# Performance work log

Hardware: AMD Instinct MI355X
Metric: run time of the kernel (lower is better)

## Reference

```python
import jax, jax.numpy as jnp
import numpy as np

B, C, H, W = 4, 256, 48, 48
NUM_HEADS = 8
HEAD_DIM = C // NUM_HEADS
LN_EPS = 1e-5


def setup_inputs() -> dict:
    key = jax.random.key(0)
    ks = jax.random.split(key, 12)
    s = 1.0 / np.sqrt(C)
    return {
        "x": jax.random.normal(ks[0], (B, C, H, W), dtype=jnp.float32),
        "context": jax.random.normal(ks[1], (B, C, H, W), dtype=jnp.float32),
        "Wq": jax.random.uniform(ks[2], (C, C), jnp.float32, -s, s),
        "bq": jax.random.uniform(ks[3], (C,), jnp.float32, -s, s),
        "Wk": jax.random.uniform(ks[4], (C, C), jnp.float32, -s, s),
        "bk": jax.random.uniform(ks[5], (C,), jnp.float32, -s, s),
        "Wv": jax.random.uniform(ks[6], (C, C), jnp.float32, -s, s),
        "bv": jax.random.uniform(ks[7], (C,), jnp.float32, -s, s),
        "Wo": jax.random.uniform(ks[8], (C, C), jnp.float32, -s, s),
        "bo": jax.random.uniform(ks[9], (C,), jnp.float32, -s, s),
        "ln_w": jnp.ones((C,), jnp.float32),
        "ln_b": jnp.zeros((C,), jnp.float32),
    }


def reference(x, context, Wq, bq, Wk, bk, Wv, bv, Wo, bo, ln_w, ln_b):
    b, c, h, w = x.shape
    S = h * w
    # [B, S, C] token layout (x.view(B,C,-1).permute(0,2,1))
    x_flat = x.reshape(b, c, S).transpose(0, 2, 1)
    ctx_flat = context.reshape(b, c, S).transpose(0, 2, 1)
    # QKV projections (torch Linear: y = x @ W.T + b)
    q = (x_flat @ Wq.T + bq).reshape(b, S, NUM_HEADS, HEAD_DIM).transpose(0, 2, 1, 3)
    k = (ctx_flat @ Wk.T + bk).reshape(b, S, NUM_HEADS, HEAD_DIM).transpose(0, 2, 1, 3)
    v = (ctx_flat @ Wv.T + bv).reshape(b, S, NUM_HEADS, HEAD_DIM).transpose(0, 2, 1, 3)
    # attention: [B, heads, S, S]
    scores = jnp.einsum("bhqd,bhkd->bhqk", q, k) / np.sqrt(HEAD_DIM)
    attn = jax.nn.softmax(scores, axis=-1)  # dropout is identity in eval mode
    attended = jnp.einsum("bhqk,bhkd->bhqd", attn, v)
    attended = attended.transpose(0, 2, 1, 3).reshape(b, S, c)
    out = attended @ Wo.T + bo
    # residual + layernorm over channel dim
    y = out + x_flat
    mu = jnp.mean(y, axis=-1, keepdims=True)
    var = jnp.var(y, axis=-1, keepdims=True)
    y = (y - mu) * jax.lax.rsqrt(var + LN_EPS) * ln_w + ln_b
    return y.transpose(0, 2, 1).reshape(b, c, h, w)
```

## Files before the change

kernel.cpp:

```cpp
#include <hip/hip_runtime.h>

#define B_ 4
#define C_ 256
#define S_ 2304
#define NH_ 8
#define HD_ 32
#define QS_L2E (0.17677669529663687f * 1.4426950408889634f)

typedef __attribute__((ext_vector_type(8))) __bf16 b16x8;
typedef __attribute__((ext_vector_type(4))) __bf16 b16x4;
typedef __attribute__((ext_vector_type(4))) float f32x4;

static __device__ __forceinline__ f32x4 mfma_bf16(b16x8 a, b16x8 b, f32x4 c) {
  return __builtin_amdgcn_mfma_f32_16x16x32_bf16(a, b, c, 0, 0, 0);
}

__global__ __launch_bounds__(256) void k_cvt(
    const float* __restrict__ x, const float* __restrict__ ctx,
    const float* __restrict__ Wq, const float* __restrict__ Wk,
    const float* __restrict__ Wv, const float* __restrict__ Wo,
    __bf16* __restrict__ xT, __bf16* __restrict__ cT,
    __bf16* __restrict__ Wb, __bf16* __restrict__ Wob) {
  const int bid = blockIdx.x, t = threadIdx.x;
  if (bid < 1152) {
    __shared__ float tile[32][33];
    const int tr = t >> 3, tc = (t & 7) * 4;
#pragma unroll
    for (int i = 0; i < 4; ++i) {
      const int tid4 = bid * 4 + i;
      const int s = tid4 / 2304;
      int r = tid4 % 2304;
      const int b = r / 576; r %= 576;
      const int ct = r / 72, st = r % 72;
      const float* src = (s == 0 ? x : ctx) + ((size_t)b * C_ + ct * 32) * S_ + st * 32;
      if (i) __syncthreads();
      f32x4 v = *(const f32x4*)(src + (size_t)tr * S_ + tc);
      tile[tr][tc] = v[0]; tile[tr][tc + 1] = v[1];
      tile[tr][tc + 2] = v[2]; tile[tr][tc + 3] = v[3];
      __syncthreads();
      __bf16* dst = (s == 0 ? xT : cT) + ((size_t)b * S_ + st * 32 + tr) * C_ + ct * 32 + tc;
      b16x4 o;
#pragma unroll
      for (int j = 0; j < 4; ++j) o[j] = (__bf16)tile[tc + j][tr];
      *(b16x4*)dst = o;
    }
  } else {
    const int bid2 = bid - 1152;
#pragma unroll
    for (int i = 0; i < 4; ++i) {
      const int wi = bid2 * 4 + i;
      const int m = wi >> 6, chunk = wi & 63;
      const float* Wsrc = m == 0 ? Wq : (m == 1 ? Wk : (m == 2 ? Wv : Wo));
      __bf16* Wdst = (m < 3) ? (Wb + m * 65536) : Wob;
      const int e0 = chunk * 1024 + t * 4;
      f32x4 v = *(const f32x4*)(Wsrc + e0);
      b16x4 o;
#pragma unroll
      for (int j = 0; j < 4; ++j) o[j] = (__bf16)v[j];
      *(b16x4*)(Wdst + e0) = o;
    }
  }
}

__global__ __launch_bounds__(256) void k_qkv(
    const __bf16* __restrict__ xT, const __bf16* __restrict__ cT,
    const __bf16* __restrict__ Wb,
    const float* __restrict__ bq, const float* __restrict__ bk, const float* __restrict__ bv,
    __bf16* __restrict__ Q, __bf16* __restrict__ Kd, __bf16* __restrict__ Vt) {
  const int iblk = threadIdx.x >> 6;
  const int lane = threadIdx.x & 63;
  const int col = lane & 15, g = lane >> 4;
  int r = blockIdx.x;
  const int p = r / 288; r %= 288;
  const int b = r / 72;
  const int s0 = (r % 72) * 32;
  const __bf16* src = (p == 0 ? xT : cT) + (size_t)b * S_ * C_;
  const __bf16* W = Wb + p * 65536;
  const float* bias = p == 0 ? bq : (p == 1 ? bk : bv);
  const int i0 = iblk * 64;

  f32x4 acc[2][4] = {};
  const __bf16* brow0 = src + (size_t)(s0 + col) * C_ + g * 8;
  const __bf16* brow1 = brow0 + 16 * C_;
  const __bf16* arow = W + (size_t)(i0 + col) * C_ + g * 8;

  b16x8 bf0 = *(const b16x8*)(brow0);
  b16x8 bf1 = *(const b16x8*)(brow1);
  b16x8 af0 = *(const b16x8*)(arow);
  b16x8 af1 = *(const b16x8*)(arow + (size_t)16 * C_);
  b16x8 af2 = *(const b16x8*)(arow + (size_t)32 * C_);
  b16x8 af3 = *(const b16x8*)(arow + (size_t)48 * C_);

  for (int kk = 0; kk < 8; ++kk) {
    const int nk = (kk + 1) * 32;
    b16x8 nbf0 = *(const b16x8*)(brow0 + nk);
    b16x8 nbf1 = *(const b16x8*)(brow1 + nk);
    b16x8 naf0 = *(const b16x8*)(arow + nk);
    b16x8 naf1 = *(const b16x8*)(arow + (size_t)16 * C_ + nk);
    b16x8 naf2 = *(const b16x8*)(arow + (size_t)32 * C_ + nk);
    b16x8 naf3 = *(const b16x8*)(arow + (size_t)48 * C_ + nk);
    __builtin_amdgcn_sched_barrier(0);
    acc[0][0] = mfma_bf16(af0, bf0, acc[0][0]);
    acc[0][1] = mfma_bf16(af1, bf0, acc[0][1]);
    acc[0][2] = mfma_bf16(af2, bf0, acc[0][2]);
    acc[0][3] = mfma_bf16(af3, bf0, acc[0][3]);
    acc[1][0] = mfma_bf16(af0, bf1, acc[1][0]);
    acc[1][1] = mfma_bf16(af1, bf1, acc[1][1]);
    acc[1][2] = mfma_bf16(af2, bf1, acc[1][2]);
    acc[1][3] = mfma_bf16(af3, bf1, acc[1][3]);
    bf0 = nbf0; bf1 = nbf1; af0 = naf0; af1 = naf1; af2 = naf2; af3 = naf3;
  }
#pragma unroll
  for (int tf = 0; tf < 2; ++tf) {
#pragma unroll
    for (int j = 0; j < 4; ++j) {
#pragma unroll
      for (int rr = 0; rr < 4; ++rr) {
        const int i = i0 + j * 16 + g * 4 + rr;
        float val = acc[tf][j][rr] + bias[i];
        const int h = i >> 5, d = i & 31;
        const size_t bh = (size_t)b * NH_ + h;
        const int tok = s0 + tf * 16 + col;
        if (p == 0)      Q[(bh * S_ + tok) * HD_ + d] = (__bf16)(val * QS_L2E);
        else if (p == 1) Kd[(bh * S_ + tok) * HD_ + d] = (__bf16)val;
        else             Vt[(bh * HD_ + d) * S_ + tok] = (__bf16)val;
      }
    }
  }
}

__global__ __launch_bounds__(192) void k_attn(
    const __bf16* __restrict__ Q, const __bf16* __restrict__ Kd,
    const __bf16* __restrict__ Vt, __bf16* __restrict__ att) {
  __shared__ float mrg[2][4][528];
  int bid = blockIdx.x;
  bid = (bid & 7) * 144 + (bid >> 3);
  const int wid = threadIdx.x >> 6;
  const int lane = threadIdx.x & 63;
  const int col = lane & 15, g = lane >> 4;
  const int bh = bid / 36;
  const int s0 = (bid % 36) * 64;
  const int b = bh >> 3, h = bh & 7;
  const __bf16* Qb = Q + (size_t)bh * S_ * HD_;
  const __bf16* Kb = Kd + (size_t)bh * S_ * HD_;
  const __bf16* Vb = Vt + (size_t)bh * HD_ * S_;

  b16x8 qfr[4];
#pragma unroll
  for (int q = 0; q < 4; ++q)
    qfr[q] = *(const b16x8*)(Qb + (size_t)(s0 + q * 16 + col) * HD_ + g * 8);
  const int kA = ((col >> 2) * 8) + (col & 3);
  const int kbeg = wid * (S_ / 3);

  b16x8 onesf;
#pragma unroll
  for (int j = 0; j < 8; ++j) onesf[j] = (__bf16)1.0f;

  f32x4 acc0[4] = {}, acc1[4] = {}, accl[4] = {};
  const f32x4 zero = {};

  const __bf16* kptr = Kb + (size_t)(kbeg + kA) * HD_ + g * 8;
  const __bf16* vptr = Vb + (size_t)col * S_ + kbeg + g * 8;

  b16x8 ka = *(const b16x8*)(kptr);
  b16x8 kb = *(const b16x8*)(kptr + 4 * HD_);
  b16x8 v0 = *(const b16x8*)(vptr);
  b16x8 v1 = *(const b16x8*)(vptr + 16 * S_);

  for (int it = 0; it < S_ / 3 / 32; ++it) {
    kptr += 32 * HD_; vptr += 32;
    b16x8 ka_n = *(const b16x8*)(kptr);
    b16x8 kb_n = *(const b16x8*)(kptr + 4 * HD_);
    b16x8 v0_n = *(const b16x8*)(vptr);
    b16x8 v1_n = *(const b16x8*)(vptr + 16 * S_);
    __builtin_amdgcn_sched_barrier(0);

#pragma unroll
    for (int q = 0; q < 4; ++q) {
      f32x4 sA = mfma_bf16(ka, qfr[q], zero);
      f32x4 sB = mfma_bf16(kb, qfr[q], zero);
      b16x8 pf;
#pragma unroll
      for (int j = 0; j < 4; ++j) {
        pf[j]     = (__bf16)__builtin_amdgcn_exp2f(sA[j]);
        pf[4 + j] = (__bf16)__builtin_amdgcn_exp2f(sB[j]);
      }
      acc0[q] = mfma_bf16(pf, v0, acc0[q]);
      acc1[q] = mfma_bf16(pf, v1, acc1[q]);
      accl[q] = mfma_bf16(pf, onesf, accl[q]);
    }
    ka = ka_n; kb = kb_n; v0 = v0_n; v1 = v1_n;
  }

  if (wid > 0) {
#pragma unroll
    for (int qt = 0; qt < 4; ++qt) {
      float* m0 = mrg[wid - 1][qt];
      *(f32x4*)(m0 + col * 16 + g * 4) = acc0[qt];
      *(f32x4*)(m0 + (col + 16) * 16 + g * 4) = acc1[qt];
      if (col == 0) *(f32x4*)(m0 + 512 + g * 4) = accl[qt];
    }
  }
  __syncthreads();
  if (wid == 0) {
#pragma unroll
    for (int qt = 0; qt < 4; ++qt) {
      const float* p0 = mrg[0][qt];
      const float* p1 = mrg[1][qt];
      f32x4 o0a = *(const f32x4*)(p0 + col * 16 + g * 4);
      f32x4 o1a = *(const f32x4*)(p0 + (col + 16) * 16 + g * 4);
      f32x4 ola = *(const f32x4*)(p0 + 512 + g * 4);
      f32x4 o0b = *(const f32x4*)(p1 + col * 16 + g * 4);
      f32x4 o1b = *(const f32x4*)(p1 + (col + 16) * 16 + g * 4);
      f32x4 olb = *(const f32x4*)(p1 + 512 + g * 4);
#pragma unroll
      for (int j = 0; j < 4; ++j) {
        const int q = g * 4 + j;
        const float inv = 1.f / (accl[qt][j] + ola[j] + olb[j]);
        const size_t obase = ((size_t)b * S_ + s0 + qt * 16 + q) * C_ + h * HD_;
        att[obase + col] = (__bf16)((acc0[qt][j] + o0a[j] + o0b[j]) * inv);
        att[obase + 16 + col] = (__bf16)((acc1[qt][j] + o1a[j] + o1b[j]) * inv);
      }
    }
  }
}

__global__ __launch_bounds__(256) void k_oln(
    const __bf16* __restrict__ att, const __bf16* __restrict__ Wob,
    const float* __restrict__ bo, const float* __restrict__ x,
    const float* __restrict__ lnw, const float* __restrict__ lnb,
    float* __restrict__ out) {
  __shared__ float part[4][2][16];
  __shared__ float lw[256], lb[256];
  const int wid = threadIdx.x >> 6;
  const int lane = threadIdx.x & 63;
  const int col = lane & 15, g = lane >> 4;
  int r = blockIdx.x;
  const int b = r / 144;
  const int s0 = (r % 144) * 16;
  const int i0 = wid * 64;
  lw[threadIdx.x] = lnw[threadIdx.x];
  lb[threadIdx.x] = lnb[threadIdx.x];

  f32x4 acc[4] = {};
  const __bf16* arow = att + ((size_t)b * S_ + s0 + col) * C_ + g * 8;
  const __bf16* wrow = Wob + (size_t)(i0 + col) * C_ + g * 8;

  b16x8 bfr = *(const b16x8*)(arow);
  b16x8 af0 = *(const b16x8*)(wrow);
  b16x8 af1 = *(const b16x8*)(wrow + (size_t)16 * C_);
  b16x8 af2 = *(const b16x8*)(wrow + (size_t)32 * C_);
  b16x8 af3 = *(const b16x8*)(wrow + (size_t)48 * C_);

  for (int kk = 0; kk < 8; ++kk) {
    const int nk = (kk + 1) * 32;
    b16x8 nbfr = *(const b16x8*)(arow + nk);
    b16x8 naf0 = *(const b16x8*)(wrow + nk);
    b16x8 naf1 = *(const b16x8*)(wrow + (size_t)16 * C_ + nk);
    b16x8 naf2 = *(const b16x8*)(wrow + (size_t)32 * C_ + nk);
    b16x8 naf3 = *(const b16x8*)(wrow + (size_t)48 * C_ + nk);
    __builtin_amdgcn_sched_barrier(0);
    acc[0] = mfma_bf16(af0, bfr, acc[0]);
    acc[1] = mfma_bf16(af1, bfr, acc[1]);
    acc[2] = mfma_bf16(af2, bfr, acc[2]);
    acc[3] = mfma_bf16(af3, bfr, acc[3]);
    bfr = nbfr; af0 = naf0; af1 = naf1; af2 = naf2; af3 = naf3;
  }
  float s = 0.f, s2 = 0.f;
#pragma unroll
  for (int j = 0; j < 4; ++j) {
#pragma unroll
    for (int rr = 0; rr < 4; ++rr) {
      const int i = i0 + j * 16 + g * 4 + rr;
      float v = acc[j][rr] + bo[i] + x[((size_t)b * C_ + i) * S_ + s0 + col];
      acc[j][rr] = v;
      s += v; s2 += v * v;
    }
  }
  s += __shfl_xor(s, 16); s2 += __shfl_xor(s2, 16);
  s += __shfl_xor(s, 32); s2 += __shfl_xor(s2, 32);
  if (g == 0) { part[wid][0][col] = s; part[wid][1][col] = s2; }
  __syncthreads();
  float st = part[0][0][col] + part[1][0][col] + part[2][0][col] + part[3][0][col];
  float st2 = part[0][1][col] + part[1][1][col] + part[2][1][col] + part[3][1][col];
  const float mu = st * (1.f / 256.f);
  const float rs = rsqrtf(st2 * (1.f / 256.f) - mu * mu + 1e-5f);
#pragma unroll
  for (int j = 0; j < 4; ++j) {
#pragma unroll
    for (int rr = 0; rr < 4; ++rr) {
      const int i = i0 + j * 16 + g * 4 + rr;
      out[((size_t)b * C_ + i) * S_ + s0 + col] = (acc[j][rr] - mu) * rs * lw[i] + lb[i];
    }
  }
}

extern "C" void kernel_launch(void* const* d_in, const int* in_sizes, int n_in,
                              void* d_out, int out_size, void* d_ws, size_t ws_size,
                              hipStream_t stream) {
  const float* x   = (const float*)d_in[0];
  const float* ctx = (const float*)d_in[1];
  const float* Wq  = (const float*)d_in[2];
  const float* bq  = (const float*)d_in[3];
  const float* Wk  = (const float*)d_in[4];
  const float* bk  = (const float*)d_in[5];
  const float* Wv  = (const float*)d_in[6];
  const float* bv  = (const float*)d_in[7];
  const float* Wo  = (const float*)d_in[8];
  const float* bo  = (const float*)d_in[9];
  const float* lnw = (const float*)d_in[10];
  const float* lnb = (const float*)d_in[11];
  float* out = (float*)d_out;

  char* ws = (char*)d_ws;
  __bf16* xT  = (__bf16*)(ws);
  __bf16* cT  = (__bf16*)(ws + 4718592);
  __bf16* Wb  = (__bf16*)(ws + 9437184);
  __bf16* Wob = (__bf16*)(ws + 9830400);
  __bf16* Kd  = (__bf16*)(ws + 9961472);
  __bf16* Vt  = (__bf16*)(ws + 14680064);
  __bf16* att = (__bf16*)(ws + 19398656);
  __bf16* Q   = (__bf16*)(ws + 24117248);

  k_cvt  <<<1216, 256, 0, stream>>>(x, ctx, Wq, Wk, Wv, Wo, xT, cT, Wb, Wob);
  k_qkv  <<< 864, 256, 0, stream>>>(xT, cT, Wb, bq, bk, bv, Q, Kd, Vt);
  k_attn <<<1152, 192, 0, stream>>>(Q, Kd, Vt, att);
  k_oln  <<< 576, 256, 0, stream>>>(att, Wob, bo, x, lnw, lnb, out);
}
```

Baseline: 191.9 us.

## Fuse input transpose into QKV GEMM, split attention keys across four waves

```diff
diff --git a/kernel.cpp b/kernel.cpp
--- a/kernel.cpp
+++ b/kernel.cpp
@@ -10,91 +10,79 @@
 typedef __attribute__((ext_vector_type(8))) __bf16 b16x8;
 typedef __attribute__((ext_vector_type(4))) __bf16 b16x4;
 typedef __attribute__((ext_vector_type(4))) float f32x4;
+typedef __attribute__((ext_vector_type(4))) unsigned u32x4;
 
 static __device__ __forceinline__ f32x4 mfma_bf16(b16x8 a, b16x8 b, f32x4 c) {
   return __builtin_amdgcn_mfma_f32_16x16x32_bf16(a, b, c, 0, 0, 0);
 }
 
-__global__ __launch_bounds__(256) void k_cvt(
-    const float* __restrict__ x, const float* __restrict__ ctx,
+__global__ __launch_bounds__(256) void k_cvtw(
     const float* __restrict__ Wq, const float* __restrict__ Wk,
     const float* __restrict__ Wv, const float* __restrict__ Wo,
-    __bf16* __restrict__ xT, __bf16* __restrict__ cT,
     __bf16* __restrict__ Wb, __bf16* __restrict__ Wob) {
-  const int bid = blockIdx.x, t = threadIdx.x;
-  if (bid < 1152) {
-    __shared__ float tile[32][33];
-    const int tr = t >> 3, tc = (t & 7) * 4;
-#pragma unroll
-    for (int i = 0; i < 4; ++i) {
-      const int tid4 = bid * 4 + i;
-      const int s = tid4 / 2304;
-      int r = tid4 % 2304;
-      const int b = r / 576; r %= 576;
-      const int ct = r / 72, st = r % 72;
-      const float* src = (s == 0 ? x : ctx) + ((size_t)b * C_ + ct * 32) * S_ + st * 32;
-      if (i) __syncthreads();
-      f32x4 v = *(const f32x4*)(src + (size_t)tr * S_ + tc);
-      tile[tr][tc] = v[0]; tile[tr][tc + 1] = v[1];
-      tile[tr][tc + 2] = v[2]; tile[tr][tc + 3] = v[3];
-      __syncthreads();
-      __bf16* dst = (s == 0 ? xT : cT) + ((size_t)b * S_ + st * 32 + tr) * C_ + ct * 32 + tc;
-      b16x4 o;
-#pragma unroll
-      for (int j = 0; j < 4; ++j) o[j] = (__bf16)tile[tc + j][tr];
-      *(b16x4*)dst = o;
-    }
+  const int e = blockIdx.x * 1024 + threadIdx.x * 4;
+  const float* s;
+  __bf16* d;
+  if (e < 196608) {
+    const int m = e >> 16;
+    s = (m == 0 ? Wq : (m == 1 ? Wk : Wv)) + (e & 65535);
+    d = Wb + e;
   } else {
-    const int bid2 = bid - 1152;
-#pragma unroll
-    for (int i = 0; i < 4; ++i) {
-      const int wi = bid2 * 4 + i;
-      const int m = wi >> 6, chunk = wi & 63;
-      const float* Wsrc = m == 0 ? Wq : (m == 1 ? Wk : (m == 2 ? Wv : Wo));
-      __bf16* Wdst = (m < 3) ? (Wb + m * 65536) : Wob;
-      const int e0 = chunk * 1024 + t * 4;
-      f32x4 v = *(const f32x4*)(Wsrc + e0);
-      b16x4 o;
-#pragma unroll
-      for (int j = 0; j < 4; ++j) o[j] = (__bf16)v[j];
-      *(b16x4*)(Wdst + e0) = o;
-    }
-  }
+    s = Wo + (e - 196608);
+    d = Wob + (e - 196608);
+  }
+  f32x4 v = *(const f32x4*)s;
+  b16x4 o;
+#pragma unroll
+  for (int j = 0; j < 4; ++j) o[j] = (__bf16)v[j];
+  *(b16x4*)d = o;
 }
 
 __global__ __launch_bounds__(256) void k_qkv(
-    const __bf16* __restrict__ xT, const __bf16* __restrict__ cT,
+    const float* __restrict__ x, const float* __restrict__ ctx,
     const __bf16* __restrict__ Wb,
     const float* __restrict__ bq, const float* __restrict__ bk, const float* __restrict__ bv,
     __bf16* __restrict__ Q, __bf16* __restrict__ Kd, __bf16* __restrict__ Vt) {
-  const int iblk = threadIdx.x >> 6;
-  const int lane = threadIdx.x & 63;
+  __shared__ __bf16 lx[33][264];
+  const int t = threadIdx.x;
+  const int iblk = t >> 6;
+  const int lane = t & 63;
   const int col = lane & 15, g = lane >> 4;
   int r = blockIdx.x;
   const int p = r / 288; r %= 288;
   const int b = r / 72;
   const int s0 = (r % 72) * 32;
-  const __bf16* src = (p == 0 ? xT : cT) + (size_t)b * S_ * C_;
+  const float* src = (p == 0 ? x : ctx) + (size_t)b * C_ * S_ + s0;
   const __bf16* W = Wb + p * 65536;
   const float* bias = p == 0 ? bq : (p == 1 ? bk : bv);
   const int i0 = iblk * 64;
-
-  f32x4 acc[2][4] = {};
-  const __bf16* brow0 = src + (size_t)(s0 + col) * C_ + g * 8;
-  const __bf16* brow1 = brow0 + 16 * C_;
   const __bf16* arow = W + (size_t)(i0 + col) * C_ + g * 8;
 
-  b16x8 bf0 = *(const b16x8*)(brow0);
-  b16x8 bf1 = *(const b16x8*)(brow1);
   b16x8 af0 = *(const b16x8*)(arow);
   b16x8 af1 = *(const b16x8*)(arow + (size_t)16 * C_);
   b16x8 af2 = *(const b16x8*)(arow + (size_t)32 * C_);
   b16x8 af3 = *(const b16x8*)(arow + (size_t)48 * C_);
 
+  {
+    const int tr = t >> 3, tc = (t & 7) * 4;
+#pragma unroll
+    for (int j = 0; j < 8; ++j) {
+      const int c = j * 32 + tr;
+      f32x4 v = *(const f32x4*)(src + (size_t)c * S_ + tc);
+#pragma unroll
+      for (int jj = 0; jj < 4; ++jj) lx[tc + jj][c] = (__bf16)v[jj];
+    }
+  }
+  __syncthreads();
+
+  f32x4 acc[2][4] = {};
+  b16x8 bf0 = *(const b16x8*)(&lx[col][g * 8]);
+  b16x8 bf1 = *(const b16x8*)(&lx[16 + col][g * 8]);
+
   for (int kk = 0; kk < 8; ++kk) {
-    const int nk = (kk + 1) * 32;
-    b16x8 nbf0 = *(const b16x8*)(brow0 + nk);
-    b16x8 nbf1 = *(const b16x8*)(brow1 + nk);
+    const int nk = ((kk + 1) & 7) * 32;
+    b16x8 nbf0 = *(const b16x8*)(&lx[col][nk + g * 8]);
+    b16x8 nbf1 = *(const b16x8*)(&lx[16 + col][nk + g * 8]);
     b16x8 naf0 = *(const b16x8*)(arow + nk);
     b16x8 naf1 = *(const b16x8*)(arow + (size_t)16 * C_ + nk);
     b16x8 naf2 = *(const b16x8*)(arow + (size_t)32 * C_ + nk);
@@ -129,10 +117,10 @@
   }
 }
 
-__global__ __launch_bounds__(192) void k_attn(
+__global__ __launch_bounds__(256) void k_attn(
     const __bf16* __restrict__ Q, const __bf16* __restrict__ Kd,
     const __bf16* __restrict__ Vt, __bf16* __restrict__ att) {
-  __shared__ float mrg[2][4][528];
+  __shared__ float mrg[3][4][528];
   int bid = blockIdx.x;
   bid = (bid & 7) * 144 + (bid >> 3);
   const int wid = threadIdx.x >> 6;
@@ -150,7 +138,7 @@
   for (int q = 0; q < 4; ++q)
     qfr[q] = *(const b16x8*)(Qb + (size_t)(s0 + q * 16 + col) * HD_ + g * 8);
   const int kA = ((col >> 2) * 8) + (col & 3);
-  const int kbeg = wid * (S_ / 3);
+  const int kbeg = wid * (S_ / 4);
 
   b16x8 onesf;
 #pragma unroll
@@ -167,7 +155,7 @@
   b16x8 v0 = *(const b16x8*)(vptr);
   b16x8 v1 = *(const b16x8*)(vptr + 16 * S_);
 
-  for (int it = 0; it < S_ / 3 / 32; ++it) {
+  for (int it = 0; it < S_ / 4 / 32; ++it) {
     kptr += 32 * HD_; vptr += 32;
     b16x8 ka_n = *(const b16x8*)(kptr);
     b16x8 kb_n = *(const b16x8*)(kptr + 4 * HD_);
@@ -179,12 +167,21 @@
     for (int q = 0; q < 4; ++q) {
       f32x4 sA = mfma_bf16(ka, qfr[q], zero);
       f32x4 sB = mfma_bf16(kb, qfr[q], zero);
-      b16x8 pf;
-#pragma unroll
-      for (int j = 0; j < 4; ++j) {
-        pf[j]     = (__bf16)__builtin_amdgcn_exp2f(sA[j]);
-        pf[4 + j] = (__bf16)__builtin_amdgcn_exp2f(sB[j]);
-      }
+      float eA0 = __builtin_amdgcn_exp2f(sA[0]);
+      float eA1 = __builtin_amdgcn_exp2f(sA[1]);
+      float eA2 = __builtin_amdgcn_exp2f(sA[2]);
+      float eA3 = __builtin_amdgcn_exp2f(sA[3]);
+      float eB0 = __builtin_amdgcn_exp2f(sB[0]);
+      float eB1 = __builtin_amdgcn_exp2f(sB[1]);
+      float eB2 = __builtin_amdgcn_exp2f(sB[2]);
+      float eB3 = __builtin_amdgcn_exp2f(sB[3]);
+      unsigned w0, w1, w2, w3;
+      asm("v_cvt_pk_bf16_f32 %0, %1, %2" : "=v"(w0) : "v"(eA0), "v"(eA1));
+      asm("v_cvt_pk_bf16_f32 %0, %1, %2" : "=v"(w1) : "v"(eA2), "v"(eA3));
+      asm("v_cvt_pk_bf16_f32 %0, %1, %2" : "=v"(w2) : "v"(eB0), "v"(eB1));
+      asm("v_cvt_pk_bf16_f32 %0, %1, %2" : "=v"(w3) : "v"(eB2), "v"(eB3));
+      u32x4 pw = {w0, w1, w2, w3};
+      b16x8 pf = __builtin_bit_cast(b16x8, pw);
       acc0[q] = mfma_bf16(pf, v0, acc0[q]);
       acc1[q] = mfma_bf16(pf, v1, acc1[q]);
       accl[q] = mfma_bf16(pf, onesf, accl[q]);
@@ -205,21 +202,21 @@
   if (wid == 0) {
 #pragma unroll
     for (int qt = 0; qt < 4; ++qt) {
-      const float* p0 = mrg[0][qt];
-      const float* p1 = mrg[1][qt];
-      f32x4 o0a = *(const f32x4*)(p0 + col * 16 + g * 4);
-      f32x4 o1a = *(const f32x4*)(p0 + (col + 16) * 16 + g * 4);
-      f32x4 ola = *(const f32x4*)(p0 + 512 + g * 4);
-      f32x4 o0b = *(const f32x4*)(p1 + col * 16 + g * 4);
-      f32x4 o1b = *(const f32x4*)(p1 + (col + 16) * 16 + g * 4);
-      f32x4 olb = *(const f32x4*)(p1 + 512 + g * 4);
+      f32x4 t0 = acc0[qt], t1 = acc1[qt], tl = accl[qt];
+#pragma unroll
+      for (int m = 0; m < 3; ++m) {
+        const float* pm = mrg[m][qt];
+        t0 += *(const f32x4*)(pm + col * 16 + g * 4);
+        t1 += *(const f32x4*)(pm + (col + 16) * 16 + g * 4);
+        tl += *(const f32x4*)(pm + 512 + g * 4);
+      }
 #pragma unroll
       for (int j = 0; j < 4; ++j) {
         const int q = g * 4 + j;
-        const float inv = 1.f / (accl[qt][j] + ola[j] + olb[j]);
+        const float inv = 1.f / tl[j];
         const size_t obase = ((size_t)b * S_ + s0 + qt * 16 + q) * C_ + h * HD_;
-        att[obase + col] = (__bf16)((acc0[qt][j] + o0a[j] + o0b[j]) * inv);
-        att[obase + 16 + col] = (__bf16)((acc1[qt][j] + o1a[j] + o1b[j]) * inv);
+        att[obase + col] = (__bf16)(t0[j] * inv);
+        att[obase + 16 + col] = (__bf16)(t1[j] * inv);
       }
     }
   }
@@ -253,7 +250,7 @@
   b16x8 af3 = *(const b16x8*)(wrow + (size_t)48 * C_);
 
   for (int kk = 0; kk < 8; ++kk) {
-    const int nk = (kk + 1) * 32;
+    const int nk = ((kk + 1) & 7) * 32;
     b16x8 nbfr = *(const b16x8*)(arow + nk);
     b16x8 naf0 = *(const b16x8*)(wrow + nk);
     b16x8 naf1 = *(const b16x8*)(wrow + (size_t)16 * C_ + nk);
@@ -313,8 +310,6 @@
   float* out = (float*)d_out;
 
   char* ws = (char*)d_ws;
-  __bf16* xT  = (__bf16*)(ws);
-  __bf16* cT  = (__bf16*)(ws + 4718592);
   __bf16* Wb  = (__bf16*)(ws + 9437184);
   __bf16* Wob = (__bf16*)(ws + 9830400);
   __bf16* Kd  = (__bf16*)(ws + 9961472);
@@ -322,8 +317,8 @@
   __bf16* att = (__bf16*)(ws + 19398656);
   __bf16* Q   = (__bf16*)(ws + 24117248);
 
-  k_cvt  <<<1216, 256, 0, stream>>>(x, ctx, Wq, Wk, Wv, Wo, xT, cT, Wb, Wob);
-  k_qkv  <<< 864, 256, 0, stream>>>(xT, cT, Wb, bq, bk, bv, Q, Kd, Vt);
-  k_attn <<<1152, 192, 0, stream>>>(Q, Kd, Vt, att);
+  k_cvtw <<< 256, 256, 0, stream>>>(Wq, Wk, Wv, Wo, Wb, Wob);
+  k_qkv  <<< 864, 256, 0, stream>>>(x, ctx, Wb, bq, bk, bv, Q, Kd, Vt);
+  k_attn <<<1152, 256, 0, stream>>>(Q, Kd, Vt, att);
   k_oln  <<< 576, 256, 0, stream>>>(att, Wob, bo, x, lnw, lnb, out);
 }
```

Result: faster. 173.9 us (-9.4%).
